# Performance work log

Measured on AMD Instinct MI355X. Metric: run time of the kernel, lower is better.

## Reference

```python
import jax, jax.numpy as jnp
import numpy as np


def _ap_class_loss(s_plus, s_minus):
    """AP rank loss for one class.

    s_plus:  [P] positive scores sorted DESCENDING (grads flow through sort gather)
    s_minus: [N] negative scores sorted ASCENDING  (grads flow through sort gather)

    The original torch code computes the optimal interleaving rank of each
    negative with a recursive quickselect divide-and-conquer. Because the
    optimal rank is monotone in the negative's score (the property the
    divide-and-conquer exploits), each negative's rank can equivalently be
    computed independently: for the negative of ascending rank j (1-indexed),
    delta_k = 1/(P*(j+k)) - 2*(s_plus[k-1] - s_minus[j-1])/(P*N),  k=1..P,
    opt_j = argmax over r in [1, P+1] of sum_{k>=r} delta_k (first max on ties),
    which is exactly opt_j() evaluated on the full range.
    """
    P = s_plus.shape[0]
    N = s_minus.shape[0]
    Pf, Nf = float(P), float(N)
    j = jnp.arange(1, N + 1, dtype=jnp.float32)[:, None]   # [N,1] ascending rank
    k = jnp.arange(1, P + 1, dtype=jnp.float32)[None, :]   # [1,P]
    # delta[m, k-1] for negative m (ascending) vs positive k (descending)
    delta = (1.0 / (j + k)) / Pf - 2.0 * (s_plus[None, :] - s_minus[:, None]) / (Pf * Nf)
    dz = jnp.concatenate([delta, jnp.zeros((N, 1), delta.dtype)], axis=1)  # [N,P+1]
    # suffix[m, u] = sum_{i>=u} dz[m, i]  (matches flip-cumsum-flip in torch)
    suffix = jnp.cumsum(dz[:, ::-1], axis=1)[:, ::-1]
    opt = 1 + jnp.argmax(suffix, axis=1)                    # [N] int in [1, P+1]
    opt_f = jax.lax.stop_gradient(opt.astype(jnp.float32))
    # r_plus[i] = 1 + |{m : opt_m <= i+1}| via cumulative histogram of opt values
    hist = jnp.zeros(P + 2, jnp.float32).at[opt].add(1.0)
    cum = jnp.cumsum(hist)
    r_plus = 1.0 + cum[1:P + 1]                             # [P], thresholds 1..P
    i_arr = jnp.arange(P, dtype=jnp.float32)
    Delta_R_R_star = 1.0 - jnp.sum((i_arr + 1.0) / (i_arr + r_plus)) / Pf
    c_plus = Nf + 2.0 - 2.0 * r_plus                        # detached in torch
    c_minus = Pf + 2.0 - 2.0 * opt_f
    F_R = jnp.dot(s_plus, c_plus) + jnp.dot(s_minus, c_minus)
    # c_plus_star = N*ones, c_minus_star = -P*ones
    F_R_star = Nf * jnp.sum(s_plus) - Pf * jnp.sum(s_minus)
    return jax.lax.stop_gradient(Delta_R_R_star) + (F_R - F_R_star) / (Pf * Nf)


def _ap_loss(scores, pos_neg):
    total = jnp.zeros((), scores.dtype)
    for c, (pos, neg) in enumerate(pos_neg):
        if pos.size == 0 or neg.size == 0:
            continue  # torch returns 0 * s_plus.sum()
        col = scores[:, c]
        sp = col[pos]
        sm = col[neg]
        sp = sp[jnp.argsort(-sp)]   # descending; detached sort idx, grad via gather
        sm = sm[jnp.argsort(sm)]    # ascending (quickselect partial sort, same pairing)
        total = total + _ap_class_loss(sp, sm)
    return total / len(pos_neg)


def setup_inputs() -> dict:
    key = jax.random.key(0)
    k1, k2 = jax.random.split(key)
    C, n_classes = 16384, 16
    scores = jax.random.normal(k1, (C, n_classes), dtype=jnp.float32)
    class_labels = jax.random.randint(k2, (C,), 0, n_classes, dtype=jnp.int32)
    return {"scores": scores, "class_labels": class_labels}


def reference(scores, class_labels):
    labels = np.asarray(class_labels)
    n_classes = scores.shape[1]
    pos_neg = [(np.nonzero(labels == c)[0], np.nonzero(labels != c)[0])
               for c in range(n_classes)]
    return _ap_loss(scores, pos_neg)
```

## Files before the change

### kernel.cpp

```cpp
#include <hip/hip_runtime.h>
#include <stdint.h>

#define C_ITEMS 16384
#define NCLS 16
#define HSTRIDE 16386
#define NB 16384
#define BSH 18

static const size_t OFF_COL  = 0;
static const size_t OFF_SPOS = 1u << 20;
static const size_t OFF_SNEG = 2u << 20;
static const size_t OFF_PACK = 3u << 20;
static const size_t OFF_HIST = 4u << 20;
static const size_t OFF_CNT  = OFF_HIST + (size_t)NCLS * HSTRIDE * 4;
static const size_t OFF_ACCS = OFF_CNT + 64;
static const size_t OFF_ACCV = OFF_ACCS + 128;
static const size_t OFF_TOT  = OFF_ACCV + 128;
static const size_t OFF_PC   = OFF_TOT + 8;
static const size_t OFF_H1   = (OFF_PC + 64 + 255) & ~(size_t)255;
static const size_t ZERO_END = OFF_H1 + ((size_t)NCLS * NB * 4);
static const size_t ZERO_BYTES = ZERO_END - OFF_HIST;
static const size_t OFF_PPK  = 6656u << 10;

__device__ __forceinline__ unsigned ordkey(float f) {
  unsigned b = __float_as_uint(f);
  return (b & 0x80000000u) ? ~b : (b | 0x80000000u);
}

__global__ void k_zero(unsigned* __restrict__ p, int n) {
  int stride = gridDim.x * blockDim.x;
  for (int t = blockIdx.x * blockDim.x + threadIdx.x; t < n; t += stride) p[t] = 0u;
}

__global__ void k_prep2(const float* __restrict__ scores, const int* __restrict__ labels,
                        float* __restrict__ col, unsigned* __restrict__ pcnt,
                        unsigned long long* __restrict__ ppk, unsigned* __restrict__ h1) {
  __shared__ unsigned lc[NCLS];
  __shared__ unsigned base[NCLS];
  int tid = threadIdx.x;
  if (tid < NCLS) lc[tid] = 0;
  __syncthreads();
  int i = blockIdx.x * 256 + tid;
  const float4* rp = (const float4*)(scores + (size_t)i * NCLS);
  float4 r0 = rp[0], r1 = rp[1], r2 = rp[2], r3 = rp[3];
  float vals[16] = {r0.x, r0.y, r0.z, r0.w, r1.x, r1.y, r1.z, r1.w,
                    r2.x, r2.y, r2.z, r2.w, r3.x, r3.y, r3.z, r3.w};
  int c = labels[i] & 15;
  unsigned loc = atomicAdd(&lc[c], 1u);
  __syncthreads();
  if (tid < NCLS) base[tid] = lc[tid] ? atomicAdd(&pcnt[tid], lc[tid]) : 0u;
  __syncthreads();
  float v = vals[c];
  ppk[(c << 14) + base[c] + loc] = ((unsigned long long)(~ordkey(v)) << 32) | (unsigned)i;
#pragma unroll
  for (int cc = 0; cc < NCLS; ++cc) {
    col[(cc << 14) + i] = vals[cc];
    if (cc != c) atomicAdd(&h1[(cc << 14) + (ordkey(vals[cc]) >> BSH)], 1u);
  }
}

#define PCAP 2048
__global__ void k_mid(unsigned* __restrict__ h1, const float* __restrict__ col,
                      const unsigned* __restrict__ pcnt,
                      const unsigned long long* __restrict__ ppk,
                      float* __restrict__ spos) {
  int b = blockIdx.x;
  int tid = threadIdx.x;
  if (b < NCLS) {
    unsigned* h = h1 + ((size_t)b << 14);
    __shared__ unsigned part[256];
    unsigned base = (unsigned)tid << 6;
    unsigned s = 0;
    for (int q = 0; q < 64; ++q) s += h[base + q];
    part[tid] = s;
    __syncthreads();
    for (int off = 1; off < 256; off <<= 1) {
      unsigned v = (tid >= off) ? part[tid - off] : 0u;
      __syncthreads();
      part[tid] += v;
      __syncthreads();
    }
    unsigned running = part[tid] - s;
    for (int q = 0; q < 64; ++q) {
      unsigned tmp = h[base + q];
      h[base + q] = running;
      running += tmp;
    }
  } else {
    int c = (b - NCLS) >> 2, s4 = (b - NCLS) & 3;
    unsigned P = pcnt[c];
    __shared__ unsigned long long pk[PCAP];
    const unsigned long long* src = ppk + ((size_t)c << 14);
    if (P <= PCAP) {
      for (unsigned t = tid; t < P; t += 256) pk[t] = src[t];
      __syncthreads();
      for (unsigned q = (unsigned)((tid << 2) + s4); q < P; q += 1024) {
        unsigned long long k64 = pk[q];
        unsigned cq = 0;
        for (unsigned t = 0; t < P; ++t) cq += (pk[t] < k64) ? 1u : 0u;
        unsigned i = (unsigned)(k64 & 0xFFFFFFFFu);
        spos[(c << 14) + cq] = col[(c << 14) + (int)i];
      }
    } else {
      for (unsigned q = (unsigned)((tid << 2) + s4); q < P; q += 1024) {
        unsigned long long k64 = src[q];
        unsigned cq = 0;
        for (unsigned t = 0; t < P; ++t) cq += (src[t] < k64) ? 1u : 0u;
        unsigned i = (unsigned)(k64 & 0xFFFFFFFFu);
        spos[(c << 14) + cq] = col[(c << 14) + (int)i];
      }
    }
  }
}

__global__ void k_scatter(const float* __restrict__ col, const int* __restrict__ labels,
                          unsigned* __restrict__ h1, unsigned* __restrict__ pack) {
  int t = blockIdx.x * 256 + threadIdx.x;
  int c = t >> 14, i = t & 16383;
  if (labels[i] != c) {
    unsigned k = ordkey(col[t]);
    unsigned p = atomicAdd(&h1[(c << 14) + (k >> BSH)], 1u);
    pack[(c << 14) + p] = (k << 14) | (unsigned)i;
  }
}

__global__ void k_rankfine(const float* __restrict__ col, const int* __restrict__ labels,
                           const unsigned* __restrict__ h1, const unsigned* __restrict__ pack,
                           float* __restrict__ sneg) {
  int t = blockIdx.x * 256 + threadIdx.x;
  int c = t >> 14, i = t & 16383;
  if (labels[i] != c) {
    float v = col[t];
    unsigned k = ordkey(v);
    unsigned b = k >> BSH;
    const unsigned* hb = h1 + ((size_t)c << 14);
    unsigned start = b ? hb[b - 1] : 0u;
    unsigned end = hb[b];
    unsigned mine = (k << 14) | (unsigned)i;
    const unsigned* pk = pack + (c << 14);
    unsigned cnt = start;
    for (unsigned q = start; q < end; ++q) cnt += (pk[q] < mine) ? 1u : 0u;
    sneg[(c << 14) + (int)cnt] = v;
  }
}

#define SCAP 2048
#define ASTEP 64
#define ABITS 6

__global__ void k_anchor(const unsigned* __restrict__ counts, const float* __restrict__ spos,
                         const float* __restrict__ sneg, unsigned* __restrict__ aopt) {
  int c = blockIdx.y;
  int P = (int)counts[c];
  int N = C_ITEMS - P;
  if (P == 0 || N == 0) return;
  int tid = threadIdx.x;
  __shared__ float sp[SCAP];
  int stageN = (P <= SCAP) ? P : 0;
  for (int t = tid; t < stageN; t += 64) sp[t] = spos[(c << 14) + t];
  __syncthreads();
  int ta = blockIdx.x * 64 + tid;
  int T = (N + ASTEP - 1) / ASTEP + 1;
  if (ta >= T) return;
  float invP = 1.0f / (float)P;
  float coef = 2.0f / ((float)P * (float)N);
  int j0 = min(ta * ASTEP, N - 1);
  float v = sneg[(c << 14) + j0];
  float a = coef * v;
  float fcnt = (float)(j0 + P + 1);
  float s = 0.0f, best = 0.0f;
  int besti = P;
  if (P <= SCAP) {
    for (int q = P - 1; q >= 0; --q) {
      float spv = sp[q];
      float r = __builtin_amdgcn_rcpf(fcnt);
      float delta = fmaf(invP, r, fmaf(-coef, spv, a));
      s += delta;
      if (s >= best) { best = s; besti = q; }
      fcnt -= 1.0f;
    }
  } else {
    const float* spg = spos + ((size_t)c << 14);
    for (int q = P - 1; q >= 0; --q) {
      float spv = spg[q];
      float r = __builtin_amdgcn_rcpf(fcnt);
      float delta = fmaf(invP, r, fmaf(-coef, spv, a));
      s += delta;
      if (s >= best) { best = s; besti = q; }
      fcnt -= 1.0f;
    }
  }
  aopt[(c << 9) + ta] = (unsigned)(besti + 1);
}

#define HCAP 2048
__global__ void k_optB(const unsigned* __restrict__ counts, const float* __restrict__ spos,
                       const float* __restrict__ sneg, const unsigned* __restrict__ aopt,
                       unsigned* __restrict__ hist, double* __restrict__ accS,
                       double* __restrict__ accV) {
  int c = blockIdx.y;
  int P = (int)counts[c];
  int N = C_ITEMS - P;
  if (P == 0 || N == 0) return;
  int tid = threadIdx.x;
  int j0 = blockIdx.x * 256 + tid;
  bool active = (j0 < N);
  __shared__ float sp[SCAP];
  __shared__ unsigned lh[HCAP];
  __shared__ double red[256];
  int stageN = (P <= SCAP) ? P : 0;
  int zn = (P + 2 <= HCAP) ? (P + 2) : 0;
  for (int t = tid; t < stageN; t += 256) sp[t] = spos[(c << 14) + t];
  for (int t = tid; t < zn; t += 256) lh[t] = 0u;
  __syncthreads();
  int opt = P + 1;
  float v = 0.0f;
  if (active) {
    v = sneg[(c << 14) + j0];
    int g = j0 >> ABITS;
    int hiA = (int)aopt[(c << 9) + g];
    if ((j0 & (ASTEP - 1)) == 0) {
      opt = hiA;
    } else {
      int loA = (int)aopt[(c << 9) + g + 1];
      int hi = min(hiA + 2, P + 1);
      int lo = max(loA - 2, 1);
      float invP = 1.0f / (float)P;
      float coef = 2.0f / ((float)P * (float)N);
      float a = coef * v;
      float s = 0.0f, best = 0.0f;
      int bestr = hi;
      float fcnt = (float)(j0 + hi);
      if (P <= SCAP) {
        for (int k = hi - 1; k >= lo; --k) {
          float spv = sp[k - 1];
          float r = __builtin_amdgcn_rcpf(fcnt);
          float delta = fmaf(invP, r, fmaf(-coef, spv, a));
          s += delta;
          if (s >= best) { best = s; bestr = k; }
          fcnt -= 1.0f;
        }
      } else {
        const float* spg = spos + ((size_t)c << 14);
        for (int k = hi - 1; k >= lo; --k) {
          float spv = spg[k - 1];
          float r = __builtin_amdgcn_rcpf(fcnt);
          float delta = fmaf(invP, r, fmaf(-coef, spv, a));
          s += delta;
          if (s >= best) { best = s; bestr = k; }
          fcnt -= 1.0f;
        }
      }
      opt = bestr;
    }
  }
  if (P + 2 <= HCAP) {
    if (active) atomicAdd(&lh[opt], 1u);
    __syncthreads();
    for (int t = tid; t < P + 2; t += 256)
      if (lh[t]) atomicAdd(&hist[c * HSTRIDE + t], lh[t]);
  } else {
    if (active) atomicAdd(&hist[c * HSTRIDE + opt], 1u);
  }
  double cm = active ? (double)(P + 2 - 2 * opt) * (double)v : 0.0;
  double sv = active ? (double)v : 0.0;
  red[tid] = cm; __syncthreads();
  for (int sh = 128; sh > 0; sh >>= 1) { if (tid < sh) red[tid] += red[tid + sh]; __syncthreads(); }
  if (tid == 0) atomicAdd(&accS[c], red[0]);
  __syncthreads();
  red[tid] = sv; __syncthreads();
  for (int sh = 128; sh > 0; sh >>= 1) { if (tid < sh) red[tid] += red[tid + sh]; __syncthreads(); }
  if (tid == 0) atomicAdd(&accV[c], red[0]);
}

__global__ void k_fin(const unsigned* __restrict__ counts, const unsigned* __restrict__ hist,
                      const float* __restrict__ spos, const double* __restrict__ accS,
                      const double* __restrict__ accV, double* __restrict__ total,
                      unsigned* __restrict__ done, float* __restrict__ out) {
  int c = blockIdx.x;
  int tid = threadIdx.x;
  int P = (int)counts[c];
  int N = C_ITEMS - P;
  __shared__ unsigned sc[256];
  __shared__ double red[256];
  double lc = 0.0;
  if (P > 0 && N > 0) {
    const unsigned* h = hist + c * HSTRIDE;
    int M = P + 1;
    int L = (M + 255) / 256;
    int o0 = 1 + tid * L;
    int o1 = min(o0 + L, P + 2);
    unsigned part = 0;
    for (int o = o0; o < o1; ++o) part += h[o];
    sc[tid] = part;
    __syncthreads();
    if (tid == 0) {
      unsigned runp = 0;
      for (int t = 0; t < 256; ++t) { unsigned tmp = sc[t]; sc[t] = runp; runp += tmp; }
    }
    __syncthreads();
    unsigned run = sc[tid];
    double a1 = 0.0, a2 = 0.0, a3 = 0.0;
    for (int o = o0; o < o1; ++o) {
      run += h[o];
      if (o <= P) {
        int k0 = o - 1;
        double rp = 1.0 + (double)run;
        double spv = (double)spos[(c << 14) + k0];
        a1 += (double)(k0 + 1) / ((double)k0 + rp);
        a2 += spv * ((double)N + 2.0 - 2.0 * rp);
        a3 += spv;
      }
    }
    red[tid] = a1; __syncthreads();
    for (int s = 128; s > 0; s >>= 1) { if (tid < s) red[tid] += red[tid + s]; __syncthreads(); }
    double r1 = red[0]; __syncthreads();
    red[tid] = a2; __syncthreads();
    for (int s = 128; s > 0; s >>= 1) { if (tid < s) red[tid] += red[tid + s]; __syncthreads(); }
    double r2 = red[0]; __syncthreads();
    red[tid] = a3; __syncthreads();
    for (int s = 128; s > 0; s >>= 1) { if (tid < s) red[tid] += red[tid + s]; __syncthreads(); }
    double r3 = red[0];
    if (tid == 0) {
      double Pd = (double)P, Nd = (double)N;
      double FR  = r2 + accS[c];
      double FRs = Nd * r3 - Pd * accV[c];
      lc = (1.0 - r1 / Pd) + (FR - FRs) / (Pd * Nd);
    }
  }
  if (tid == 0) {
    if (P > 0 && N > 0) atomicAdd(total, lc);
    __threadfence();
    unsigned d = atomicAdd(done, 1u);
    if (d == NCLS - 1) {
      double t = atomicAdd(total, 0.0);
      out[0] = (float)(t / (double)NCLS);
    }
  }
}

extern "C" void kernel_launch(void* const* d_in, const int* in_sizes, int n_in,
                              void* d_out, int out_size, void* d_ws, size_t ws_size,
                              hipStream_t stream) {
  (void)in_sizes; (void)n_in; (void)out_size; (void)ws_size;
  const float* scores = (const float*)d_in[0];
  const int* labels = (const int*)d_in[1];
  float* out = (float*)d_out;
  char* ws = (char*)d_ws;
  float* col      = (float*)(ws + OFF_COL);
  float* spos     = (float*)(ws + OFF_SPOS);
  float* sneg     = (float*)(ws + OFF_SNEG);
  unsigned* pack  = (unsigned*)(ws + OFF_PACK);
  unsigned* hist  = (unsigned*)(ws + OFF_HIST);
  unsigned* done  = (unsigned*)(ws + OFF_CNT);
  double* accS    = (double*)(ws + OFF_ACCS);
  double* accV    = (double*)(ws + OFF_ACCV);
  double* total   = (double*)(ws + OFF_TOT);
  unsigned* pcnt  = (unsigned*)(ws + OFF_PC);
  unsigned* h1    = (unsigned*)(ws + OFF_H1);
  unsigned long long* ppk = (unsigned long long*)(ws + OFF_PPK);
  unsigned* aopt  = (unsigned*)(ws + OFF_PPK);

  int zn = (int)(ZERO_BYTES / 4);
  k_zero<<<512, 256, 0, stream>>>(hist, zn);
  k_prep2<<<64, 256, 0, stream>>>(scores, labels, col, pcnt, ppk, h1);
  k_mid<<<80, 256, 0, stream>>>(h1, col, pcnt, ppk, spos);
  k_scatter<<<1024, 256, 0, stream>>>(col, labels, h1, pack);
  k_rankfine<<<1024, 256, 0, stream>>>(col, labels, h1, pack, sneg);
  k_anchor<<<dim3(5, NCLS), 64, 0, stream>>>(pcnt, spos, sneg, aopt);
  k_optB<<<dim3(64, NCLS), 256, 0, stream>>>(pcnt, spos, sneg, aopt, hist, accS, accV);
  k_fin<<<NCLS, 256, 0, stream>>>(pcnt, hist, spos, accS, accV, total, done, out);
}
```

Measured before the change: 237.0 us.

## Widen negative radix buckets and split prep into element-parallel kernels

The coarse histogram for negatives grows from 16K to 64K buckets (BSH 18 to 16), so each bucket holds fewer items and the quadratic within-bucket rank count in k_rankfine gets shorter. The prep kernel is split into an element-parallel transpose plus histogram kernel (1024 blocks) and a separate kernel that packs the positives. k_mid now uses 1024-thread blocks, one per class, for both the scan and the positive sort. In exchange the histogram to zero and scan is four times larger, there is one extra launch, and the pack key now keeps only 16 bits of the score key plus the index.

```diff
diff --git a/kernel.cpp b/kernel.cpp
--- a/kernel.cpp
+++ b/kernel.cpp
@@ -4,8 +4,8 @@
 #define C_ITEMS 16384
 #define NCLS 16
 #define HSTRIDE 16386
-#define NB 16384
-#define BSH 18
+#define NB 65536
+#define BSH 16
 
 static const size_t OFF_COL  = 0;
 static const size_t OFF_SPOS = 1u << 20;
@@ -20,7 +20,7 @@
 static const size_t OFF_H1   = (OFF_PC + 64 + 255) & ~(size_t)255;
 static const size_t ZERO_END = OFF_H1 + ((size_t)NCLS * NB * 4);
 static const size_t ZERO_BYTES = ZERO_END - OFF_HIST;
-static const size_t OFF_PPK  = 6656u << 10;
+static const size_t OFF_PPK  = 10u << 20;
 
 __device__ __forceinline__ unsigned ordkey(float f) {
   unsigned b = __float_as_uint(f);
@@ -32,49 +32,50 @@
   for (int t = blockIdx.x * blockDim.x + threadIdx.x; t < n; t += stride) p[t] = 0u;
 }
 
-__global__ void k_prep2(const float* __restrict__ scores, const int* __restrict__ labels,
-                        float* __restrict__ col, unsigned* __restrict__ pcnt,
-                        unsigned long long* __restrict__ ppk, unsigned* __restrict__ h1) {
+__global__ void k_prep(const float* __restrict__ scores, const int* __restrict__ labels,
+                       float* __restrict__ col, unsigned* __restrict__ h1) {
+  int t = blockIdx.x * 256 + threadIdx.x;
+  float v = scores[t];
+  int i = t >> 4, c = t & 15;
+  col[(c << 14) | i] = v;
+  if (labels[i] != c)
+    atomicAdd(&h1[(c << 16) + (ordkey(v) >> BSH)], 1u);
+}
+
+__global__ void k_posc(const float* __restrict__ scores, const int* __restrict__ labels,
+                       unsigned* __restrict__ pcnt, unsigned long long* __restrict__ ppk) {
   __shared__ unsigned lc[NCLS];
   __shared__ unsigned base[NCLS];
   int tid = threadIdx.x;
   if (tid < NCLS) lc[tid] = 0;
   __syncthreads();
   int i = blockIdx.x * 256 + tid;
-  const float4* rp = (const float4*)(scores + (size_t)i * NCLS);
-  float4 r0 = rp[0], r1 = rp[1], r2 = rp[2], r3 = rp[3];
-  float vals[16] = {r0.x, r0.y, r0.z, r0.w, r1.x, r1.y, r1.z, r1.w,
-                    r2.x, r2.y, r2.z, r2.w, r3.x, r3.y, r3.z, r3.w};
   int c = labels[i] & 15;
+  float v = scores[i * NCLS + c];
   unsigned loc = atomicAdd(&lc[c], 1u);
   __syncthreads();
   if (tid < NCLS) base[tid] = lc[tid] ? atomicAdd(&pcnt[tid], lc[tid]) : 0u;
   __syncthreads();
-  float v = vals[c];
   ppk[(c << 14) + base[c] + loc] = ((unsigned long long)(~ordkey(v)) << 32) | (unsigned)i;
-#pragma unroll
-  for (int cc = 0; cc < NCLS; ++cc) {
-    col[(cc << 14) + i] = vals[cc];
-    if (cc != c) atomicAdd(&h1[(cc << 14) + (ordkey(vals[cc]) >> BSH)], 1u);
-  }
 }
 
 #define PCAP 2048
-__global__ void k_mid(unsigned* __restrict__ h1, const float* __restrict__ col,
-                      const unsigned* __restrict__ pcnt,
-                      const unsigned long long* __restrict__ ppk,
-                      float* __restrict__ spos) {
+__global__ __launch_bounds__(1024) void k_mid(
+    unsigned* __restrict__ h1, const float* __restrict__ col,
+    const unsigned* __restrict__ pcnt, const unsigned long long* __restrict__ ppk,
+    float* __restrict__ spos) {
   int b = blockIdx.x;
   int tid = threadIdx.x;
+  __shared__ unsigned part[1024];
+  __shared__ unsigned long long pk[PCAP];
   if (b < NCLS) {
-    unsigned* h = h1 + ((size_t)b << 14);
-    __shared__ unsigned part[256];
+    unsigned* h = h1 + ((size_t)b << 16);
     unsigned base = (unsigned)tid << 6;
     unsigned s = 0;
     for (int q = 0; q < 64; ++q) s += h[base + q];
     part[tid] = s;
     __syncthreads();
-    for (int off = 1; off < 256; off <<= 1) {
+    for (int off = 1; off < 1024; off <<= 1) {
       unsigned v = (tid >= off) ? part[tid - off] : 0u;
       __syncthreads();
       part[tid] += v;
@@ -87,14 +88,13 @@
       running += tmp;
     }
   } else {
-    int c = (b - NCLS) >> 2, s4 = (b - NCLS) & 3;
+    int c = b - NCLS;
     unsigned P = pcnt[c];
-    __shared__ unsigned long long pk[PCAP];
     const unsigned long long* src = ppk + ((size_t)c << 14);
     if (P <= PCAP) {
-      for (unsigned t = tid; t < P; t += 256) pk[t] = src[t];
+      for (unsigned t = tid; t < P; t += 1024) pk[t] = src[t];
       __syncthreads();
-      for (unsigned q = (unsigned)((tid << 2) + s4); q < P; q += 1024) {
+      for (unsigned q = tid; q < P; q += 1024) {
         unsigned long long k64 = pk[q];
         unsigned cq = 0;
         for (unsigned t = 0; t < P; ++t) cq += (pk[t] < k64) ? 1u : 0u;
@@ -102,7 +102,7 @@
         spos[(c << 14) + cq] = col[(c << 14) + (int)i];
       }
     } else {
-      for (unsigned q = (unsigned)((tid << 2) + s4); q < P; q += 1024) {
+      for (unsigned q = tid; q < P; q += 1024) {
         unsigned long long k64 = src[q];
         unsigned cq = 0;
         for (unsigned t = 0; t < P; ++t) cq += (src[t] < k64) ? 1u : 0u;
@@ -119,8 +119,8 @@
   int c = t >> 14, i = t & 16383;
   if (labels[i] != c) {
     unsigned k = ordkey(col[t]);
-    unsigned p = atomicAdd(&h1[(c << 14) + (k >> BSH)], 1u);
-    pack[(c << 14) + p] = (k << 14) | (unsigned)i;
+    unsigned p = atomicAdd(&h1[(c << 16) + (k >> BSH)], 1u);
+    pack[(c << 14) + p] = (k << 16) | (unsigned)i;
   }
 }
 
@@ -133,10 +133,10 @@
     float v = col[t];
     unsigned k = ordkey(v);
     unsigned b = k >> BSH;
-    const unsigned* hb = h1 + ((size_t)c << 14);
+    const unsigned* hb = h1 + ((size_t)c << 16);
     unsigned start = b ? hb[b - 1] : 0u;
     unsigned end = hb[b];
-    unsigned mine = (k << 14) | (unsigned)i;
+    unsigned mine = (k << 16) | (unsigned)i;
     const unsigned* pk = pack + (c << 14);
     unsigned cnt = start;
     for (unsigned q = start; q < end; ++q) cnt += (pk[q] < mine) ? 1u : 0u;
@@ -362,9 +362,10 @@
   unsigned* aopt  = (unsigned*)(ws + OFF_PPK);
 
   int zn = (int)(ZERO_BYTES / 4);
-  k_zero<<<512, 256, 0, stream>>>(hist, zn);
-  k_prep2<<<64, 256, 0, stream>>>(scores, labels, col, pcnt, ppk, h1);
-  k_mid<<<80, 256, 0, stream>>>(h1, col, pcnt, ppk, spos);
+  k_zero<<<1024, 256, 0, stream>>>(hist, zn);
+  k_prep<<<1024, 256, 0, stream>>>(scores, labels, col, h1);
+  k_posc<<<64, 256, 0, stream>>>(scores, labels, pcnt, ppk);
+  k_mid<<<32, 1024, 0, stream>>>(h1, col, pcnt, ppk, spos);
   k_scatter<<<1024, 256, 0, stream>>>(col, labels, h1, pack);
   k_rankfine<<<1024, 256, 0, stream>>>(col, labels, h1, pack, sneg);
   k_anchor<<<dim3(5, NCLS), 64, 0, stream>>>(pcnt, spos, sneg, aopt);
```

After: 199.2 us. -16.0%, faster.
